# Kernel optimization log

Measured on AMD Instinct MI355X. Metric: run time of the kernel, lower is better.

The kernel has to match this reference:

```python
import jax, jax.numpy as jnp
import numpy as np
from jax import lax

B, C, H, W = 2, 256, 128, 128
NC, NP = 80, 9  # num_classes, num_points (3x3 dcn kernel)
PAD = 1


def conv2d(x, w, b=None, pad=1):
    out = lax.conv_general_dilated(x, w, (1, 1), [(pad, pad), (pad, pad)],
                                   dimension_numbers=('NCHW', 'OIHW', 'NCHW'))
    if b is not None:
        out = out + b[None, :, None, None]
    return out


def bilinear_sample(img_bhwc, py, px):
    # zero-padded bilinear sampling; py/px: [B,H,W] float coords
    Hi, Wi = img_bhwc.shape[1], img_bhwc.shape[2]
    y0 = jnp.floor(py)
    x0 = jnp.floor(px)
    wy1 = py - y0
    wx1 = px - x0

    def gather(yc, xc, w):
        valid = (yc >= 0) & (yc <= Hi - 1) & (xc >= 0) & (xc <= Wi - 1)
        yi = jnp.clip(yc, 0, Hi - 1).astype(jnp.int32)
        xi = jnp.clip(xc, 0, Wi - 1).astype(jnp.int32)
        v = jax.vmap(lambda im, yy, xx: im[yy, xx])(img_bhwc, yi, xi)  # [B,H,W,C]
        return v * (w * valid)[..., None]

    return (gather(y0, x0, (1 - wy1) * (1 - wx1)) + gather(y0, x0 + 1, (1 - wy1) * wx1)
            + gather(y0 + 1, x0, wy1 * (1 - wx1)) + gather(y0 + 1, x0 + 1, wy1 * wx1))


def deform_conv(x, offset, weight, mask=None, pad=1):
    # x: [B,C,H,W]; offset: [B,2K,H,W] interleaved (dy,dx) per kernel point;
    # mask: [B,K,H,W] or None (modulated DCN multiplies sampled value by mask as-is)
    kh, kw = weight.shape[2], weight.shape[3]
    xb = jnp.transpose(x, (0, 2, 3, 1))  # [B,H,W,C]
    gy, gx = jnp.meshgrid(jnp.arange(x.shape[2], dtype=x.dtype),
                          jnp.arange(x.shape[3], dtype=x.dtype), indexing='ij')
    acc = 0.
    for k in range(kh * kw):  # fixed structural loop over 9 kernel points
        ky, kx = k // kw, k % kw
        py = gy[None] + (ky - pad) + offset[:, 2 * k]
        px = gx[None] + (kx - pad) + offset[:, 2 * k + 1]
        val = bilinear_sample(xb, py, px)  # [B,H,W,C]
        if mask is not None:
            val = val * mask[:, k][..., None]
        acc = acc + jnp.einsum('bhwc,oc->bohw', val, weight[:, :, ky, kx])
    return acc


def setup_inputs() -> dict:
    key = jax.random.key(0)
    ks = jax.random.split(key, 16)
    d = {"x": jax.random.normal(ks[0], (B, C, H, W), jnp.float32)}

    def w(k, shape):
        return jax.random.normal(k, shape, jnp.float32) * 0.01

    i = 1
    for j in range(3):
        d[f"cls_w{j}"] = w(ks[i], (C, C, 3, 3)); i += 1
        d[f"cls_b{j}"] = jnp.zeros((C,), jnp.float32)
        d[f"reg_w{j}"] = w(ks[i], (C, C, 3, 3)); i += 1
        d[f"reg_b{j}"] = jnp.zeros((C,), jnp.float32)
    d["init_conv_w"] = w(ks[i], (C, C, 3, 3)); i += 1
    d["init_conv_b"] = jnp.zeros((C,), jnp.float32)
    d["init_out_w"] = w(ks[i], (3 * NP, C, 1, 1)); i += 1
    d["init_out_b"] = jnp.zeros((3 * NP,), jnp.float32)
    d["dcn_cls_w"] = w(ks[i], (C, C, 3, 3)); i += 1  # ModulatedDeformConv (bias=False)
    d["cls_out_w"] = w(ks[i], (NC, C, 1, 1)); i += 1
    d["cls_out_b"] = jnp.full((NC,), -4.59511985013459, jnp.float32)  # bias_init_with_prob(0.01)
    d["dcn_ref_w"] = w(ks[i], (C, C, 3, 3)); i += 1  # DeformConv (bias=False)
    d["ref_out_w"] = w(ks[i], (2 * NP, C, 1, 1)); i += 1
    d["ref_out_b"] = jnp.zeros((2 * NP,), jnp.float32)
    return d


def reference(x, cls_w0, cls_b0, reg_w0, reg_b0, cls_w1, cls_b1, reg_w1, reg_b1,
              cls_w2, cls_b2, reg_w2, reg_b2, init_conv_w, init_conv_b,
              init_out_w, init_out_b, dcn_cls_w, cls_out_w, cls_out_b,
              dcn_ref_w, ref_out_w, ref_out_b):
    relu = jax.nn.relu
    cls_feat = x
    for wgt, b in ((cls_w0, cls_b0), (cls_w1, cls_b1), (cls_w2, cls_b2)):
        cls_feat = relu(conv2d(cls_feat, wgt, b, 1))
    pts_feat = x
    for wgt, b in ((reg_w0, reg_b0), (reg_w1, reg_b1), (reg_w2, reg_b2)):
        pts_feat = relu(conv2d(pts_feat, wgt, b, 1))

    pts_out_init = conv2d(relu(conv2d(pts_feat, init_conv_w, init_conv_b, 1)),
                          init_out_w, init_out_b, 0)  # [B,27,H,W]
    o1, o2, mask = (pts_out_init[:, :NP], pts_out_init[:, NP:2 * NP],
                    pts_out_init[:, 2 * NP:])
    offset = jnp.concatenate([o1, o2], axis=1)  # dcn_offset (points_init = 0)

    cls_out = conv2d(relu(deform_conv(cls_feat, offset, dcn_cls_w, mask)),
                     cls_out_w, cls_out_b, 0)
    pts_out_refine = conv2d(relu(deform_conv(pts_feat, offset, dcn_ref_w)),
                            ref_out_w, ref_out_b, 0)
    pts_out_refine = pts_out_refine + lax.stop_gradient(offset)

    # pts2wh_offsets
    pts = pts_out_refine.reshape(B, NP, 2, H, W)
    pts_mean = pts.mean(axis=1, keepdims=True)          # [B,1,2,H,W]
    wh = jnp.abs(pts + pts_mean).max(axis=1)            # [B,2,H,W]
    reg = pts_mean[:, 0]                                # [B,2,H,W]
    return (cls_out, wh, reg)
```

## Files before the change

### kernel.cpp

```cpp
#include <hip/hip_runtime.h>

#define Bn 2
#define Cn 256
#define Hn 128
#define Wn 128
#define HWn 16384
#define NCn 80

typedef __attribute__((ext_vector_type(4))) float f32x4;
typedef __attribute__((ext_vector_type(8))) short bf16x8;

__device__ __forceinline__ float blo(unsigned u) {
    union { unsigned u; float f; } x; x.u = u << 16; return x.f;
}
__device__ __forceinline__ float braw(unsigned u) {
    union { unsigned u; float f; } x; x.u = u; return x.f;
}
__device__ __forceinline__ unsigned short f2bf(float f) {
    union { float f; unsigned u; } x; x.f = f;
    unsigned u = x.u + 0x7fffu + ((x.u >> 16) & 1u);
    return (unsigned short)(u >> 16);
}
__device__ __forceinline__ unsigned pk2bf(float e0, float e1) {
    unsigned r;
    asm("v_cvt_pk_bf16_f32 %0, %1, %2" : "=v"(r) : "v"(e0), "v"(e1));
    return r;
}

#define GLOAD16(gp, lp) __builtin_amdgcn_global_load_lds( \
    (__attribute__((address_space(1))) unsigned int*)(gp), \
    (__attribute__((address_space(3))) unsigned int*)(lp), 16, 0, 0)

__global__ __launch_bounds__(256) void xinK(const float* __restrict__ x,
                                            unsigned short* __restrict__ o) {
    __shared__ float tb[32][33];
    const int b = blockIdx.z;
    const int hw0 = blockIdx.x * 32, c0 = blockIdx.y * 32;
    const int tx = threadIdx.x & 31, ty = threadIdx.x >> 5;
    const float* ip = x + ((size_t)(b * Cn + c0)) * HWn + hw0;
#pragma unroll
    for (int r = 0; r < 4; ++r) tb[ty + 8 * r][tx] = ip[(size_t)(ty + 8 * r) * HWn + tx];
    __syncthreads();
    unsigned short* op = o + ((size_t)(b * HWn + hw0)) * Cn + c0;
#pragma unroll
    for (int r = 0; r < 4; ++r) op[(size_t)(ty + 8 * r) * Cn + tx] = f2bf(tb[tx][ty + 8 * r]);
}

struct RPtrs { const float* w3[9]; const float* wh[3]; };
__global__ __launch_bounds__(256) void repackAllK(RPtrs rp,
                                                  unsigned short* __restrict__ dst3,
                                                  unsigned short* __restrict__ dstH,
                                                  unsigned short* __restrict__ zb) {
    if (blockIdx.x < 2304) {
        if (blockIdx.x == 0) { zb[threadIdx.x] = 0; zb[256 + threadIdx.x] = 0; }
        const int t = blockIdx.x * 256 + threadIdx.x;
        const int widx = t >> 16;
        const int r = t & 65535;
        const float* s = rp.w3[widx] + (size_t)r * 9;
        float v[9];
#pragma unroll
        for (int k = 0; k < 9; ++k) v[k] = s[k];
        unsigned short* d = dst3 + (size_t)widx * 589824 + r;
#pragma unroll
        for (int k = 0; k < 9; ++k) d[(size_t)k * 65536] = f2bf(v[k]);
    } else {
        const int t = (blockIdx.x - 2304) * 256 + threadIdx.x;
        const int ic = t & 255, row = t >> 8;
        int which, oc, OC;
        if (row < 32)       { which = 0; oc = row;       OC = 27; }
        else if (row < 128) { which = 1; oc = row - 32;  OC = 80; }
        else                { which = 2; oc = row - 128; OC = 18; }
        dstH[t] = (oc < OC) ? f2bf(rp.wh[which][(size_t)oc * Cn + ic]) : (unsigned short)0;
    }
}

struct CJobs {
    const unsigned short* feat[2];
    const unsigned short* W[2];
    const float* bias[2];
    unsigned short* out[2];
};
__global__ __launch_bounds__(256, 2) void convGemm(CJobs jobs,
                                                   const unsigned short* __restrict__ zb) {
    const int jz = blockIdx.z;
    const unsigned short* feat = jobs.feat[jz];
    const unsigned short* Wp = jobs.W[jz];
    const float* bias = jobs.bias[jz];
    unsigned short* outp = jobs.out[jz];

    __shared__ __align__(16) unsigned short lA[2][8192];
    __shared__ __align__(16) unsigned short lB[2][8192];
    const int tid = threadIdx.x;
    const int l = tid & 63, w = tid >> 6;
    const int w_oc = w & 1, w_px = w >> 1;
    const int ry = (blockIdx.x & 7) * 32 + (blockIdx.x >> 3);
    const int b = ry >> 7, y = ry & 127;
    const int oc0 = blockIdx.y * 128;
    const int lr = l & 15, lg = l >> 4;

    int rI[4], cI[4], dI[4];
#pragma unroll
    for (int i = 0; i < 4; ++i) {
        int ps = (i * 4 + w) * 64 + l;
        rI[i] = ps >> 3;
        cI[i] = ((ps & 7) ^ (rI[i] & 7)) * 8;
        dI[i] = (i * 4 + w) * 512;
    }

    f32x4 acc[4][4];
#pragma unroll
    for (int i = 0; i < 4; ++i)
#pragma unroll
        for (int j = 0; j < 4; ++j) acc[i][j] = (f32x4){0.f, 0.f, 0.f, 0.f};

    auto stage = [&](int p, int bufIdx) {
        const int k = p >> 2, c0 = (p & 3) * 64;
        const int dy = k / 3 - 1, dx = k % 3 - 1;
        const int yy = y + dy;
        const bool vy = (unsigned)yy < (unsigned)Hn;
        const size_t fbase = ((size_t)(b * Hn + yy)) * Wn;
        const unsigned short* wk = Wp + (size_t)k * 65536 + (size_t)oc0 * Cn + c0;
        unsigned short* la = lA[bufIdx];
        unsigned short* lb = lB[bufIdx];
#pragma unroll
        for (int i = 0; i < 4; ++i)
            GLOAD16(wk + rI[i] * Cn + cI[i], la + dI[i]);
#pragma unroll
        for (int i = 0; i < 4; ++i) {
            const int pxs = rI[i] + dx;
            const unsigned short* g = (vy && (unsigned)pxs < (unsigned)Wn)
                ? feat + ((fbase + pxs) * Cn + c0 + cI[i])
                : zb;
            GLOAD16(g, lb + dI[i]);
        }
    };

    stage(0, 0);
    __syncthreads();

#pragma unroll 1
    for (int p = 0; p < 36; ++p) {
        const int cur = p & 1;
        if (p < 35) stage(p + 1, cur ^ 1);
        const unsigned short* la = lA[cur];
        const unsigned short* lb = lB[cur];
#pragma unroll
        for (int h = 0; h < 2; ++h) {
            const int ch = h * 4 + lg;
            bf16x8 av[4], bv[4];
#pragma unroll
            for (int fm = 0; fm < 4; ++fm) {
                const int row = w_oc * 64 + fm * 16 + lr;
                av[fm] = *(const bf16x8*)&la[row * 64 + ((ch ^ (row & 7)) * 8)];
            }
#pragma unroll
            for (int fn = 0; fn < 4; ++fn) {
                const int row = w_px * 64 + fn * 16 + lr;
                bv[fn] = *(const bf16x8*)&lb[row * 64 + ((ch ^ (row & 7)) * 8)];
            }
#pragma unroll
            for (int fm = 0; fm < 4; ++fm)
#pragma unroll
                for (int fn = 0; fn < 4; ++fn)
                    acc[fm][fn] = __builtin_amdgcn_mfma_f32_16x16x32_bf16(
                        av[fm], bv[fn], acc[fm][fn], 0, 0, 0);
        }
        __syncthreads();
    }

#pragma unroll
    for (int fm = 0; fm < 4; ++fm) {
        const int ocb = oc0 + w_oc * 64 + fm * 16 + lg * 4;
        const float b0 = bias[ocb], b1 = bias[ocb + 1], b2 = bias[ocb + 2], b3 = bias[ocb + 3];
#pragma unroll
        for (int fn = 0; fn < 4; ++fn) {
            const int px = w_px * 64 + fn * 16 + lr;
            f32x4 v = acc[fm][fn];
            uint2 st;
            st.x = pk2bf(fmaxf(v[0] + b0, 0.f), fmaxf(v[1] + b1, 0.f));
            st.y = pk2bf(fmaxf(v[2] + b2, 0.f), fmaxf(v[3] + b3, 0.f));
            *(uint2*)&outp[((size_t)ry * Wn + px) * Cn + ocb] = st;
        }
    }
}

struct DJobs {
    const unsigned short* feat[2];
    const unsigned short* W[2];
    unsigned short* out[2];
    int mask[2];
};
__global__ __launch_bounds__(512, 4) void dcnGemm(DJobs jobs,
                                                  const float* __restrict__ o27) {
    const int jz = blockIdx.x >> 9;
    const unsigned short* feat = jobs.feat[jz];
    const unsigned short* Wp = jobs.W[jz];
    unsigned short* outp = jobs.out[jz];
    const bool HASMASK = jobs.mask[jz] != 0;

    __shared__ __align__(16) unsigned short lA[2][16384];
    __shared__ __align__(16) unsigned short lB[2][4096];
    const int tid = threadIdx.x;
    const int l = tid & 63, w = tid >> 6;
    const int w_oc = w & 3, w_px = w >> 2;
    const int lb_ = blockIdx.x & 511;
    const int g = (lb_ & 7) * 64 + (lb_ >> 3);
    const int ry = g >> 1, st = g & 1;
    const int b = ry >> 7, y = ry & 127;
    const int x0 = st * 64;
    const int lr = l & 15, lg = l >> 4;

    int rIA[4], cIA[4], dIA[4];
#pragma unroll
    for (int i = 0; i < 4; ++i) {
        int ps = (i * 8 + w) * 64 + l;
        rIA[i] = ps >> 3;
        cIA[i] = ((ps & 7) ^ (rIA[i] & 7)) * 8;
        dIA[i] = (i * 8 + w) * 512;
    }

    const int sp = tid >> 3;
    const int pc = tid & 7;
    const int xg = x0 + sp;
    const int wslot = sp * 64 + ((pc ^ (sp & 7)) * 8);

    const float* ob = o27 + (size_t)b * 27 * HWn + y * Wn + xg;
    const unsigned short* fb = feat + (size_t)b * HWn * Cn;

    f32x4 acc[4][2];
#pragma unroll
    for (int i = 0; i < 4; ++i)
#pragma unroll
        for (int j = 0; j < 2; ++j) acc[i][j] = (f32x4){0.f, 0.f, 0.f, 0.f};

    int ci0, ci1, ci2, ci3;
    float cw0, cw1, cw2, cw3;
    float pofy, pofx, pom;

    auto sampFromRegs = [&](int k) {
        const float py = (float)(y + k / 3 - 1) + pofy;
        const float px = (float)(xg + k % 3 - 1) + pofx;
        const float y0f = floorf(py), x0f = floorf(px);
        const float wy1 = py - y0f, wx1 = px - x0f;
        const int iy0 = (int)y0f, ix0 = (int)x0f;
        const int iy1 = iy0 + 1, ix1 = ix0 + 1;
        const bool vy0 = (unsigned)iy0 < (unsigned)Hn, vy1 = (unsigned)iy1 < (unsigned)Hn;
        const bool vx0 = (unsigned)ix0 < (unsigned)Wn, vx1 = (unsigned)ix1 < (unsigned)Wn;
        const int yc0 = min(max(iy0, 0), Hn - 1), yc1 = min(max(iy1, 0), Hn - 1);
        const int xc0 = min(max(ix0, 0), Wn - 1), xc1 = min(max(ix1, 0), Wn - 1);
        cw0 = (vy0 && vx0) ? (1.f - wy1) * (1.f - wx1) * pom : 0.f;
        cw1 = (vy0 && vx1) ? (1.f - wy1) * wx1 * pom : 0.f;
        cw2 = (vy1 && vx0) ? wy1 * (1.f - wx1) * pom : 0.f;
        cw3 = (vy1 && vx1) ? wy1 * wx1 * pom : 0.f;
        ci0 = (yc0 * Wn + xc0) * Cn;
        ci1 = (yc0 * Wn + xc1) * Cn;
        ci2 = (yc1 * Wn + xc0) * Cn;
        ci3 = (yc1 * Wn + xc1) * Cn;
    };
    auto prefOff = [&](int k) {
        pofy = ob[(size_t)(2 * k) * HWn];
        pofx = ob[(size_t)(2 * k + 1) * HWn];
        pom = HASMASK ? ob[(size_t)(18 + k) * HWn] : 1.f;
    };

    int4 q0, q1, q2, q3;
    auto cornerLoads = [&](int p) {
        const int cb = (p & 3) * 64 + pc * 8;
        q0 = *(const int4*)(fb + ci0 + cb);
        q1 = *(const int4*)(fb + ci1 + cb);
        q2 = *(const int4*)(fb + ci2 + cb);
        q3 = *(const int4*)(fb + ci3 + cb);
    };
    auto stageA = [&](int p, int bufIdx) {
        const int k = p >> 2, c0 = (p & 3) * 64;
        const unsigned short* wk = Wp + (size_t)k * 65536 + c0;
        unsigned short* la = lA[bufIdx];
#pragma unroll
        for (int i = 0; i < 4; ++i)
            GLOAD16(wk + rIA[i] * Cn + cIA[i], la + dIA[i]);
    };
    auto interpWrite = [&](int bufIdx) {
        unsigned uu[4];
#pragma unroll
        for (int jj = 0; jj < 4; ++jj) {
            const unsigned a0 = ((const unsigned*)&q0)[jj];
            const unsigned a1 = ((const unsigned*)&q1)[jj];
            const unsigned a2 = ((const unsigned*)&q2)[jj];
            const unsigned a3 = ((const unsigned*)&q3)[jj];
            float e0 = cw0 * blo(a0) + cw1 * blo(a1) + cw2 * blo(a2) + cw3 * blo(a3);
            float e1 = cw0 * braw(a0) + cw1 * braw(a1) + cw2 * braw(a2) + cw3 * braw(a3);
            uu[jj] = pk2bf(e0, e1);
        }
        int4 pk; pk.x = uu[0]; pk.y = uu[1]; pk.z = uu[2]; pk.w = uu[3];
        *(int4*)&lB[bufIdx][wslot] = pk;
    };

    prefOff(0);
    sampFromRegs(0);
    cornerLoads(0);
    stageA(0, 0);
    interpWrite(0);
    prefOff(1);
    __syncthreads();

#pragma unroll 1
    for (int p = 0; p < 36; ++p) {
        const int cur = p & 1;
        if (p < 35) {
            if (((p + 1) & 3) == 0) sampFromRegs((p + 1) >> 2);
            cornerLoads(p + 1);
            stageA(p + 1, cur ^ 1);
            if ((p & 3) == 1 && (p >> 2) < 8) prefOff((p >> 2) + 2);
        }
        const unsigned short* la = lA[cur];
        const unsigned short* lb = lB[cur];
#pragma unroll
        for (int h = 0; h < 2; ++h) {
            const int ch = h * 4 + lg;
            bf16x8 av[4], bv[2];
#pragma unroll
            for (int fm = 0; fm < 4; ++fm) {
                const int row = w_oc * 64 + fm * 16 + lr;
                av[fm] = *(const bf16x8*)&la[row * 64 + ((ch ^ (row & 7)) * 8)];
            }
#pragma unroll
            for (int fn = 0; fn < 2; ++fn) {
                const int row = w_px * 32 + fn * 16 + lr;
                bv[fn] = *(const bf16x8*)&lb[row * 64 + ((ch ^ (row & 7)) * 8)];
            }
#pragma unroll
            for (int fm = 0; fm < 4; ++fm)
#pragma unroll
                for (int fn = 0; fn < 2; ++fn)
                    acc[fm][fn] = __builtin_amdgcn_mfma_f32_16x16x32_bf16(
                        av[fm], bv[fn], acc[fm][fn], 0, 0, 0);
        }
        if (p < 35) interpWrite(cur ^ 1);
        __syncthreads();
    }

#pragma unroll
    for (int fm = 0; fm < 4; ++fm) {
        const int oc = w_oc * 64 + fm * 16 + lg * 4;
#pragma unroll
        for (int fn = 0; fn < 2; ++fn) {
            const int px = x0 + w_px * 32 + fn * 16 + lr;
            f32x4 v = acc[fm][fn];
            uint2 stv;
            stv.x = pk2bf(fmaxf(v[0], 0.f), fmaxf(v[1], 0.f));
            stv.y = pk2bf(fmaxf(v[2], 0.f), fmaxf(v[3], 0.f));
            *(uint2*)&outp[((size_t)ry * Wn + px) * Cn + oc] = stv;
        }
    }
}


template <int OC, int PM, bool ADD, bool POST>
__device__ __forceinline__ void headBody(int bx,
                                         const unsigned short* __restrict__ feat,
                                         const unsigned short* __restrict__ Wp,
                                         const float* __restrict__ bias,
                                         float* __restrict__ out,
                                         const float* __restrict__ add, int addC,
                                         float* __restrict__ reg,
                                         unsigned short* lA, unsigned short* lB,
                                         float (*lR)[128]) {
    constexpr int MF = PM / 16;
    constexpr int NA = PM * 8 / 256;
    const int tid = threadIdx.x;
    const int l = tid & 63, w = tid >> 6;
    const int ry = (bx & 7) * 32 + (bx >> 3);
    const int b = ry >> 7, y = ry & 127;
    const int lr = l & 15, lg = l >> 4;

    int rIA[NA], cIA[NA], dIA[NA];
#pragma unroll
    for (int i = 0; i < NA; ++i) {
        int ps = (i * 4 + w) * 64 + l;
        rIA[i] = ps >> 3;
        cIA[i] = ((ps & 7) ^ (rIA[i] & 7)) * 8;
        dIA[i] = (i * 4 + w) * 512;
    }
    int rIB[4], cIB[4], dIB[4];
#pragma unroll
    for (int i = 0; i < 4; ++i) {
        int ps = (i * 4 + w) * 64 + l;
        rIB[i] = ps >> 3;
        cIB[i] = ((ps & 7) ^ (rIB[i] & 7)) * 8;
        dIB[i] = (i * 4 + w) * 512;
    }

    f32x4 acc[MF][2];
#pragma unroll
    for (int i = 0; i < MF; ++i)
#pragma unroll
        for (int j = 0; j < 2; ++j) acc[i][j] = (f32x4){0.f, 0.f, 0.f, 0.f};

    const unsigned short* frow = feat + ((size_t)ry * Wn) * Cn;

#pragma unroll 1
    for (int cc = 0; cc < 4; ++cc) {
        const int c0 = cc * 64;
#pragma unroll
        for (int i = 0; i < NA; ++i)
            GLOAD16(Wp + (size_t)rIA[i] * Cn + c0 + cIA[i], &lA[dIA[i]]);
#pragma unroll
        for (int i = 0; i < 4; ++i)
            GLOAD16(frow + (size_t)rIB[i] * Cn + c0 + cIB[i], &lB[dIB[i]]);
        __syncthreads();
#pragma unroll
        for (int h = 0; h < 2; ++h) {
            const int ch = h * 4 + lg;
            bf16x8 av[MF], bv[2];
#pragma unroll
            for (int fm = 0; fm < MF; ++fm) {
                const int row = fm * 16 + lr;
                av[fm] = *(const bf16x8*)&lA[row * 64 + ((ch ^ (row & 7)) * 8)];
            }
#pragma unroll
            for (int fn = 0; fn < 2; ++fn) {
                const int row = w * 32 + fn * 16 + lr;
                bv[fn] = *(const bf16x8*)&lB[row * 64 + ((ch ^ (row & 7)) * 8)];
            }
#pragma unroll
            for (int fm = 0; fm < MF; ++fm)
#pragma unroll
                for (int fn = 0; fn < 2; ++fn)
                    acc[fm][fn] = __builtin_amdgcn_mfma_f32_16x16x32_bf16(
                        av[fm], bv[fn], acc[fm][fn], 0, 0, 0);
        }
        __syncthreads();
    }

    if (!POST) {
#pragma unroll
        for (int fm = 0; fm < MF; ++fm) {
            const int ocb = fm * 16 + lg * 4;
            if (ocb >= OC) break;
#pragma unroll
            for (int j = 0; j < 4; ++j) {
                const int oc = ocb + j;
                if (oc >= OC) break;
                const float bs = bias[oc];
#pragma unroll
                for (int fn = 0; fn < 2; ++fn) {
                    const int px = w * 32 + fn * 16 + lr;
                    float r = acc[fm][fn][j] + bs;
                    if (ADD) r += add[((size_t)(b * addC + oc)) * HWn + y * Wn + px];
                    out[((size_t)(b * OC + oc)) * HWn + y * Wn + px] = r;
                }
            }
        }
    } else {
#pragma unroll
        for (int fm = 0; fm < MF; ++fm) {
            const int ocb = fm * 16 + lg * 4;
#pragma unroll
            for (int j = 0; j < 4; ++j) {
                const int oc = ocb + j;
                if (oc < 18) {
                    const float bs = bias[oc];
#pragma unroll
                    for (int fn = 0; fn < 2; ++fn) {
                        const int px = w * 32 + fn * 16 + lr;
                        float r = acc[fm][fn][j] + bs
                                + add[((size_t)(b * addC + oc)) * HWn + y * Wn + px];
                        lR[oc][px] = r;
                    }
                }
            }
        }
        __syncthreads();
        if (tid < 128) {
            const int px = tid;
            float v[18];
#pragma unroll
            for (int c = 0; c < 18; ++c) v[c] = lR[c][px];
            float s0 = 0.f, s1 = 0.f;
#pragma unroll
            for (int q = 0; q < 9; ++q) { s0 += v[2 * q]; s1 += v[2 * q + 1]; }
            float m0 = s0 * (1.f / 9.f), m1 = s1 * (1.f / 9.f);
            float w0 = 0.f, w1 = 0.f;
#pragma unroll
            for (int q = 0; q < 9; ++q) {
                w0 = fmaxf(w0, fabsf(v[2 * q] + m0));
                w1 = fmaxf(w1, fabsf(v[2 * q + 1] + m1));
            }
            const size_t hw = (size_t)y * Wn + px;
            out[(size_t)(b * 2 + 0) * HWn + hw] = w0;
            out[(size_t)(b * 2 + 1) * HWn + hw] = w1;
            reg[(size_t)(b * 2 + 0) * HWn + hw] = m0;
            reg[(size_t)(b * 2 + 1) * HWn + hw] = m1;
        }
    }
}

__global__ __launch_bounds__(256, 2) void head27K(const unsigned short* __restrict__ feat,
                                                  const unsigned short* __restrict__ Wp,
                                                  const float* __restrict__ bias,
                                                  float* __restrict__ out) {
    __shared__ __align__(16) unsigned short sA[32 * 64];
    __shared__ __align__(16) unsigned short sB[128 * 64];
    headBody<27, 32, false, false>(blockIdx.x, feat, Wp, bias, out,
                                   nullptr, 0, nullptr, sA, sB, nullptr);
}

__global__ __launch_bounds__(256, 2) void headTailK(const unsigned short* __restrict__ f80,
                                                    const unsigned short* __restrict__ W80,
                                                    const float* __restrict__ b80,
                                                    float* __restrict__ out80,
                                                    const unsigned short* __restrict__ f18,
                                                    const unsigned short* __restrict__ W18,
                                                    const float* __restrict__ b18,
                                                    const float* __restrict__ add27,
                                                    float* __restrict__ wh,
                                                    float* __restrict__ reg) {
    __shared__ __align__(16) unsigned short sA[96 * 64];
    __shared__ __align__(16) unsigned short sB[128 * 64];
    __shared__ float sR[18][128];
    if (blockIdx.x < 256) {
        headBody<80, 96, false, false>(blockIdx.x, f80, W80, b80, out80,
                                       nullptr, 0, nullptr, sA, sB, nullptr);
    } else {
        headBody<18, 32, true, true>(blockIdx.x - 256, f18, W18, b18, wh,
                                     add27, 27, reg, sA, sB, sR);
    }
}

extern "C" void kernel_launch(void* const* d_in, const int* in_sizes, int n_in,
                              void* d_out, int out_size, void* d_ws, size_t ws_size,
                              hipStream_t stream) {
    const float* x           = (const float*)d_in[0];
    const float* cls_w0      = (const float*)d_in[1];
    const float* cls_b0      = (const float*)d_in[2];
    const float* reg_w0      = (const float*)d_in[3];
    const float* reg_b0      = (const float*)d_in[4];
    const float* cls_w1      = (const float*)d_in[5];
    const float* cls_b1      = (const float*)d_in[6];
    const float* reg_w1      = (const float*)d_in[7];
    const float* reg_b1      = (const float*)d_in[8];
    const float* cls_w2      = (const float*)d_in[9];
    const float* cls_b2      = (const float*)d_in[10];
    const float* reg_w2      = (const float*)d_in[11];
    const float* reg_b2      = (const float*)d_in[12];
    const float* init_conv_w = (const float*)d_in[13];
    const float* init_conv_b = (const float*)d_in[14];
    const float* init_out_w  = (const float*)d_in[15];
    const float* init_out_b  = (const float*)d_in[16];
    const float* dcn_cls_w   = (const float*)d_in[17];
    const float* cls_out_w   = (const float*)d_in[18];
    const float* cls_out_b   = (const float*)d_in[19];
    const float* dcn_ref_w   = (const float*)d_in[20];
    const float* ref_out_w   = (const float*)d_in[21];
    const float* ref_out_b   = (const float*)d_in[22];

    float* out = (float*)d_out;

    char* ws = (char*)d_ws;
    const size_t IMG = (size_t)Bn * HWn * Cn * sizeof(unsigned short);
    unsigned short* B0 = (unsigned short*)ws; ws += IMG;
    unsigned short* B1 = (unsigned short*)ws; ws += IMG;
    unsigned short* B2 = (unsigned short*)ws; ws += IMG;
    unsigned short* B3 = (unsigned short*)ws; ws += IMG;
    float* O27 = (float*)ws; ws += (size_t)Bn * 27 * HWn * sizeof(float);
    const size_t WSZ = (size_t)9 * Cn * Cn;
    unsigned short* Wpk = (unsigned short*)ws; ws += 9 * WSZ * sizeof(unsigned short);
    unsigned short* WhAll = (unsigned short*)ws; ws += 160 * Cn * sizeof(unsigned short);
    unsigned short* ZB = (unsigned short*)ws;  ws += 1024;

    unsigned short* W_cls0 = Wpk + 0 * WSZ;
    unsigned short* W_cls1 = Wpk + 1 * WSZ;
    unsigned short* W_cls2 = Wpk + 2 * WSZ;
    unsigned short* W_reg0 = Wpk + 3 * WSZ;
    unsigned short* W_reg1 = Wpk + 4 * WSZ;
    unsigned short* W_reg2 = Wpk + 5 * WSZ;
    unsigned short* W_init = Wpk + 6 * WSZ;
    unsigned short* W_dcls = Wpk + 7 * WSZ;
    unsigned short* W_dref = Wpk + 8 * WSZ;
    unsigned short* Wh27 = WhAll;
    unsigned short* Wh80 = WhAll + 32 * Cn;
    unsigned short* Wh18 = WhAll + 128 * Cn;

    const dim3 blk(256);
    const dim3 xgrd(512, 8, Bn);

    RPtrs rp;
    rp.w3[0] = cls_w0; rp.w3[1] = cls_w1; rp.w3[2] = cls_w2;
    rp.w3[3] = reg_w0; rp.w3[4] = reg_w1; rp.w3[5] = reg_w2;
    rp.w3[6] = init_conv_w; rp.w3[7] = dcn_cls_w; rp.w3[8] = dcn_ref_w;
    rp.wh[0] = init_out_w; rp.wh[1] = cls_out_w; rp.wh[2] = ref_out_w;
    repackAllK<<<2464, blk, 0, stream>>>(rp, Wpk, WhAll, ZB);
    xinK<<<xgrd, blk, 0, stream>>>(x, B0);

    CJobs j;
    j.feat[0] = B0; j.W[0] = W_cls0; j.bias[0] = cls_b0; j.out[0] = B1;
    j.feat[1] = B0; j.W[1] = W_reg0; j.bias[1] = reg_b0; j.out[1] = B2;
    convGemm<<<dim3(256, 2, 2), blk, 0, stream>>>(j, ZB);
    j.feat[0] = B1; j.W[0] = W_cls1; j.bias[0] = cls_b1; j.out[0] = B3;
    j.feat[1] = B2; j.W[1] = W_reg1; j.bias[1] = reg_b1; j.out[1] = B0;
    convGemm<<<dim3(256, 2, 2), blk, 0, stream>>>(j, ZB);
    j.feat[0] = B3; j.W[0] = W_cls2; j.bias[0] = cls_b2; j.out[0] = B1;
    j.feat[1] = B0; j.W[1] = W_reg2; j.bias[1] = reg_b2; j.out[1] = B2;
    convGemm<<<dim3(256, 2, 2), blk, 0, stream>>>(j, ZB);
    j.feat[0] = B2; j.W[0] = W_init; j.bias[0] = init_conv_b; j.out[0] = B3;
    convGemm<<<dim3(256, 2, 1), blk, 0, stream>>>(j, ZB);
    head27K<<<256, blk, 0, stream>>>(B3, Wh27, init_out_b, O27);
    DJobs dj;
    dj.feat[0] = B1; dj.W[0] = W_dcls; dj.out[0] = B0; dj.mask[0] = 1;
    dj.feat[1] = B2; dj.W[1] = W_dref; dj.out[1] = B3; dj.mask[1] = 0;
    dcnGemm<<<1024, dim3(512), 0, stream>>>(dj, O27);
    headTailK<<<512, blk, 0, stream>>>(
        B0, Wh80, cls_out_b, out,
        B3, Wh18, ref_out_b, O27,
        out + (size_t)Bn * NCn * HWn,
        out + (size_t)Bn * NCn * HWn + (size_t)Bn * 2 * HWn);
}
```

Before: 567.8 us.

## Deepen deformable gather pipeline to prefetch corner loads two stages ahead

The bilinear corner gathers for the deformable conv are now issued two pipeline stages ahead, using two register sets (A/B) and a separate next-point coordinate/weight set computed early. The goal is to hide global gather latency behind more MFMA work rather than one iteration. In exchange it raises register pressure (eight int4 plus extra indices/weights), which may lower occupancy, and the index/weight swap timing is delicate.

New measurement: 869.9 us. 1.53x slower.

```diff
diff --git a/kernel.cpp b/kernel.cpp
--- a/kernel.cpp
+++ b/kernel.cpp
@@ -235,9 +235,12 @@
 
     int ci0, ci1, ci2, ci3;
     float cw0, cw1, cw2, cw3;
+    int ni0, ni1, ni2, ni3;
+    float nw0, nw1, nw2, nw3;
     float pofy, pofx, pom;
 
-    auto sampFromRegs = [&](int k) {
+    auto sampTo = [&](int k, int& o0, int& o1, int& o2, int& o3,
+                      float& u0, float& u1, float& u2, float& u3) {
         const float py = (float)(y + k / 3 - 1) + pofy;
         const float px = (float)(xg + k % 3 - 1) + pofx;
         const float y0f = floorf(py), x0f = floorf(px);
@@ -248,14 +251,14 @@
         const bool vx0 = (unsigned)ix0 < (unsigned)Wn, vx1 = (unsigned)ix1 < (unsigned)Wn;
         const int yc0 = min(max(iy0, 0), Hn - 1), yc1 = min(max(iy1, 0), Hn - 1);
         const int xc0 = min(max(ix0, 0), Wn - 1), xc1 = min(max(ix1, 0), Wn - 1);
-        cw0 = (vy0 && vx0) ? (1.f - wy1) * (1.f - wx1) * pom : 0.f;
-        cw1 = (vy0 && vx1) ? (1.f - wy1) * wx1 * pom : 0.f;
-        cw2 = (vy1 && vx0) ? wy1 * (1.f - wx1) * pom : 0.f;
-        cw3 = (vy1 && vx1) ? wy1 * wx1 * pom : 0.f;
-        ci0 = (yc0 * Wn + xc0) * Cn;
-        ci1 = (yc0 * Wn + xc1) * Cn;
-        ci2 = (yc1 * Wn + xc0) * Cn;
-        ci3 = (yc1 * Wn + xc1) * Cn;
+        u0 = (vy0 && vx0) ? (1.f - wy1) * (1.f - wx1) * pom : 0.f;
+        u1 = (vy0 && vx1) ? (1.f - wy1) * wx1 * pom : 0.f;
+        u2 = (vy1 && vx0) ? wy1 * (1.f - wx1) * pom : 0.f;
+        u3 = (vy1 && vx1) ? wy1 * wx1 * pom : 0.f;
+        o0 = (yc0 * Wn + xc0) * Cn;
+        o1 = (yc0 * Wn + xc1) * Cn;
+        o2 = (yc1 * Wn + xc0) * Cn;
+        o3 = (yc1 * Wn + xc1) * Cn;
     };
     auto prefOff = [&](int k) {
         pofy = ob[(size_t)(2 * k) * HWn];
@@ -263,14 +266,32 @@
         pom = HASMASK ? ob[(size_t)(18 + k) * HWn] : 1.f;
     };
 
-    int4 q0, q1, q2, q3;
-    auto cornerLoads = [&](int p) {
-        const int cb = (p & 3) * 64 + pc * 8;
-        q0 = *(const int4*)(fb + ci0 + cb);
-        q1 = *(const int4*)(fb + ci1 + cb);
-        q2 = *(const int4*)(fb + ci2 + cb);
-        q3 = *(const int4*)(fb + ci3 + cb);
-    };
+    int4 qA0, qA1, qA2, qA3;
+    int4 qB0, qB1, qB2, qB3;
+
+#define DISSUE(Q0, Q1, Q2, Q3, I0, I1, I2, I3, CBI) do { \
+        const int cb_ = (CBI) * 64 + pc * 8; \
+        Q0 = *(const int4*)(fb + (I0) + cb_); \
+        Q1 = *(const int4*)(fb + (I1) + cb_); \
+        Q2 = *(const int4*)(fb + (I2) + cb_); \
+        Q3 = *(const int4*)(fb + (I3) + cb_); \
+    } while (0)
+
+#define DINTERP(Q0, Q1, Q2, Q3, BUF) do { \
+        unsigned uu[4]; \
+        _Pragma("unroll") for (int jj = 0; jj < 4; ++jj) { \
+            const unsigned a0 = ((const unsigned*)&Q0)[jj]; \
+            const unsigned a1 = ((const unsigned*)&Q1)[jj]; \
+            const unsigned a2 = ((const unsigned*)&Q2)[jj]; \
+            const unsigned a3 = ((const unsigned*)&Q3)[jj]; \
+            float e0 = cw0 * blo(a0) + cw1 * blo(a1) + cw2 * blo(a2) + cw3 * blo(a3); \
+            float e1 = cw0 * braw(a0) + cw1 * braw(a1) + cw2 * braw(a2) + cw3 * braw(a3); \
+            uu[jj] = pk2bf(e0, e1); \
+        } \
+        int4 pk_; pk_.x = uu[0]; pk_.y = uu[1]; pk_.z = uu[2]; pk_.w = uu[3]; \
+        *(int4*)&lB[BUF][wslot] = pk_; \
+    } while (0)
+
     auto stageA = [&](int p, int bufIdx) {
         const int k = p >> 2, c0 = (p & 3) * 64;
         const unsigned short* wk = Wp + (size_t)k * 65536 + c0;
@@ -279,64 +300,66 @@
         for (int i = 0; i < 4; ++i)
             GLOAD16(wk + rIA[i] * Cn + cIA[i], la + dIA[i]);
     };
-    auto interpWrite = [&](int bufIdx) {
-        unsigned uu[4];
-#pragma unroll
-        for (int jj = 0; jj < 4; ++jj) {
-            const unsigned a0 = ((const unsigned*)&q0)[jj];
-            const unsigned a1 = ((const unsigned*)&q1)[jj];
-            const unsigned a2 = ((const unsigned*)&q2)[jj];
-            const unsigned a3 = ((const unsigned*)&q3)[jj];
-            float e0 = cw0 * blo(a0) + cw1 * blo(a1) + cw2 * blo(a2) + cw3 * blo(a3);
-            float e1 = cw0 * braw(a0) + cw1 * braw(a1) + cw2 * braw(a2) + cw3 * braw(a3);
-            uu[jj] = pk2bf(e0, e1);
-        }
-        int4 pk; pk.x = uu[0]; pk.y = uu[1]; pk.z = uu[2]; pk.w = uu[3];
-        *(int4*)&lB[bufIdx][wslot] = pk;
-    };
+
+#define DMFMA(BUF) do { \
+        const unsigned short* la_ = lA[BUF]; \
+        const unsigned short* lb2_ = lB[BUF]; \
+        _Pragma("unroll") for (int h = 0; h < 2; ++h) { \
+            const int ch = h * 4 + lg; \
+            bf16x8 av[4], bv[2]; \
+            _Pragma("unroll") for (int fm = 0; fm < 4; ++fm) { \
+                const int row = w_oc * 64 + fm * 16 + lr; \
+                av[fm] = *(const bf16x8*)&la_[row * 64 + ((ch ^ (row & 7)) * 8)]; } \
+            _Pragma("unroll") for (int fn = 0; fn < 2; ++fn) { \
+                const int row = w_px * 32 + fn * 16 + lr; \
+                bv[fn] = *(const bf16x8*)&lb2_[row * 64 + ((ch ^ (row & 7)) * 8)]; } \
+            _Pragma("unroll") for (int fm = 0; fm < 4; ++fm) \
+                _Pragma("unroll") for (int fn = 0; fn < 2; ++fn) \
+                    acc[fm][fn] = __builtin_amdgcn_mfma_f32_16x16x32_bf16( \
+                        av[fm], bv[fn], acc[fm][fn], 0, 0, 0); \
+        } \
+    } while (0)
 
     prefOff(0);
-    sampFromRegs(0);
-    cornerLoads(0);
+    sampTo(0, ci0, ci1, ci2, ci3, cw0, cw1, cw2, cw3);
+    DISSUE(qA0, qA1, qA2, qA3, ci0, ci1, ci2, ci3, 0);
     stageA(0, 0);
-    interpWrite(0);
+    DINTERP(qA0, qA1, qA2, qA3, 0);
+    DISSUE(qB0, qB1, qB2, qB3, ci0, ci1, ci2, ci3, 1);
     prefOff(1);
     __syncthreads();
 
 #pragma unroll 1
     for (int p = 0; p < 36; ++p) {
         const int cur = p & 1;
+        const int pm4 = p & 3;
         if (p < 35) {
-            if (((p + 1) & 3) == 0) sampFromRegs((p + 1) >> 2);
-            cornerLoads(p + 1);
+            if (pm4 == 1) {
+                const int kn = (p >> 2) + 1;
+                if (kn <= 8) sampTo(kn, ni0, ni1, ni2, ni3, nw0, nw1, nw2, nw3);
+                if ((p >> 2) + 2 <= 8) prefOff((p >> 2) + 2);
+            }
+            if (p < 34) {
+                if (pm4 == 2) {
+                    if (cur == 0) DISSUE(qA0, qA1, qA2, qA3, ni0, ni1, ni2, ni3, (p + 2) & 3);
+                    else          DISSUE(qB0, qB1, qB2, qB3, ni0, ni1, ni2, ni3, (p + 2) & 3);
+                } else {
+                    if (cur == 0) DISSUE(qA0, qA1, qA2, qA3, ci0, ci1, ci2, ci3, (p + 2) & 3);
+                    else          DISSUE(qB0, qB1, qB2, qB3, ci0, ci1, ci2, ci3, (p + 2) & 3);
+                }
+            }
             stageA(p + 1, cur ^ 1);
-            if ((p & 3) == 1 && (p >> 2) < 8) prefOff((p >> 2) + 2);
-        }
-        const unsigned short* la = lA[cur];
-        const unsigned short* lb = lB[cur];
-#pragma unroll
-        for (int h = 0; h < 2; ++h) {
-            const int ch = h * 4 + lg;
-            bf16x8 av[4], bv[2];
-#pragma unroll
-            for (int fm = 0; fm < 4; ++fm) {
-                const int row = w_oc * 64 + fm * 16 + lr;
-                av[fm] = *(const bf16x8*)&la[row * 64 + ((ch ^ (row & 7)) * 8)];
-            }
-#pragma unroll
-            for (int fn = 0; fn < 2; ++fn) {
-                const int row = w_px * 32 + fn * 16 + lr;
-                bv[fn] = *(const bf16x8*)&lb[row * 64 + ((ch ^ (row & 7)) * 8)];
-            }
-#pragma unroll
-            for (int fm = 0; fm < 4; ++fm)
-#pragma unroll
-                for (int fn = 0; fn < 2; ++fn)
-                    acc[fm][fn] = __builtin_amdgcn_mfma_f32_16x16x32_bf16(
-                        av[fm], bv[fn], acc[fm][fn], 0, 0, 0);
-        }
-        if (p < 35) interpWrite(cur ^ 1);
+        }
+        DMFMA(cur);
+        if (p < 35) {
+            if (cur == 0) DINTERP(qB0, qB1, qB2, qB3, 1);
+            else          DINTERP(qA0, qA1, qA2, qA3, 0);
+        }
         __syncthreads();
+        if (pm4 == 2 && (p >> 2) < 8) {
+            ci0 = ni0; ci1 = ni1; ci2 = ni2; ci3 = ni3;
+            cw0 = nw0; cw1 = nw1; cw2 = nw2; cw3 = nw3;
+        }
     }
 
 #pragma unroll
@@ -352,8 +375,10 @@
             *(uint2*)&outp[((size_t)ry * Wn + px) * Cn + oc] = stv;
         }
     }
-}
-
+#undef DISSUE
+#undef DINTERP
+#undef DMFMA
+}
 
 template <int OC, int PM, bool ADD, bool POST>
 __device__ __forceinline__ void headBody(int bx,
```
